# Optimization experiments

Measured on AMD Instinct MI355X. Metric: run time of the kernel, lower is better.

Reference implementation:

```python
import jax, jax.numpy as jnp
import numpy as np
from jax import lax

LEA, STE, GRA = 8, 8, 8
C_DIM = LEA + STE + GRA          # 24
AUX_DIM = 5
IN_DIM = C_DIM + AUX_DIM         # 29


def setup_inputs() -> dict:
    key = jax.random.key(0)
    ks = jax.random.split(key, 12)
    B, T = 1024, 366
    X = jax.random.uniform(ks[0], (B, T, 4), dtype=jnp.float32)
    ORY = jax.random.uniform(ks[1], (B, T, 7), dtype=jnp.float32)
    W_redis = jax.random.normal(ks[2], (C_DIM * C_DIM, IN_DIM), dtype=jnp.float32)
    b_redis = jax.random.normal(ks[3], (C_DIM * C_DIM,), dtype=jnp.float32)
    W_part = jax.random.normal(ks[4], (C_DIM, IN_DIM), dtype=jnp.float32)
    b_part = jax.random.normal(ks[5], (C_DIM,), dtype=jnp.float32)
    W_cons = jax.random.normal(ks[6], (C_DIM, IN_DIM), dtype=jnp.float32)
    b_cons = jax.random.normal(ks[7], (C_DIM,), dtype=jnp.float32)
    W_assim = jax.random.normal(ks[8], (1, IN_DIM), dtype=jnp.float32)
    b_assim = jax.random.normal(ks[9], (1,), dtype=jnp.float32)
    c2a_par = jnp.ones((C_DIM,), dtype=jnp.float32)
    g2y_par = jnp.ones((GRA,), dtype=jnp.float32)
    return dict(X=X, ORY=ORY, W_redis=W_redis, b_redis=b_redis,
                W_part=W_part, b_part=b_part, W_cons=W_cons, b_cons=b_cons,
                W_assim=W_assim, b_assim=b_assim, c2a_par=c2a_par, g2y_par=g2y_par)


def _redis_prior():
    # ones over C_cell part, zeros over aux except index -4 (rad) = 1
    p = jnp.concatenate([jnp.ones(C_DIM, jnp.float32), jnp.zeros(AUX_DIM, jnp.float32)])
    return p.at[IN_DIM - 4].set(1.0)


def _forward(X, ORY, W_redis, b_redis, W_part, b_part, W_cons, b_cons,
             W_assim, b_assim, c2a_par, g2y_par):
    B, T, _ = X.shape
    # ---- preprocessing ----
    N_cum = jnp.cumsum(X[:, :, 3], axis=-1)[..., None]          # [B,T,1]
    t_ave = jnp.mean(X[:, :, 1:3], axis=-1, keepdims=True)       # [B,T,1]
    dvs = ORY[:, :, :1]
    rad = X[:, :, 0:1]
    tmax = X[:, :, 1:2]
    tmin = X[:, :, 2:3]
    FRPAR = 0.5
    eff = 0.54 - (jnp.clip(t_ave * 50.0, 10.0, 40.0) - 10.0) / 30.0 * (0.54 - 0.36)
    R2C_par = (40000.0 / 20000.0) * FRPAR * eff / 3.6 * (12.0 / 44.0)
    C_potential = rad * R2C_par                                  # [B,T,1]
    AUX = jnp.concatenate([dvs, rad, tmax, tmin, N_cum], axis=-1)  # [B,T,5]

    redis_prior = _redis_prior()
    # all other input priors are ones, all output priors are zeros -> no-ops

    def redis_gate(x):
        z = (x * redis_prior) @ W_redis.T + b_redis
        return jax.nn.softmax(z.reshape(-1, C_DIM, C_DIM), axis=-1)

    def step(C_cell, ts):
        aux_t, cpot_t = ts                                       # [B,5], [B,1]
        x = jnp.concatenate([C_cell, aux_t], axis=1)             # [B,29]
        assim = jax.nn.sigmoid(x @ W_assim.T + b_assim)          # [B,1]
        part = jax.nn.softmax(x @ W_part.T + b_part, axis=-1)    # [B,24]
        cons = jax.nn.sigmoid(x @ W_cons.T + b_cons)             # [B,24]
        redis = redis_gate(x)                                    # [B,24,24]
        C_in = assim * cpot_t                                    # [B,1]
        C_cell = C_cell + C_in * part
        C_cell = C_cell * (1.0 - cons)
        C_cell = jnp.einsum('bi,bij->bj', C_cell, redis)
        x2 = jnp.concatenate([C_cell, aux_t], axis=1)
        redis2 = redis_gate(x2)
        C_conv = jnp.einsum('bi,bij->bj', C_cell, redis2)
        return C_cell, (C_cell, C_conv)

    aux_seq = jnp.transpose(AUX[:, :T - 1, :], (1, 0, 2))        # [T-1,B,5]
    cpot_seq = jnp.transpose(C_potential[:, :T - 1, :], (1, 0, 2))
    C0 = jnp.zeros((B, C_DIM), X.dtype)
    _, (C_all, C_conv_all) = lax.scan(step, C0, (aux_seq, cpot_seq))
    C_cell_all = jnp.transpose(C_all, (1, 0, 2))                 # [B,T-1,24]
    C_cell_convergence_all = jnp.transpose(C_conv_all, (1, 0, 2))

    pai = jnp.sum(jnp.abs(C_cell_all * c2a_par), axis=2, keepdims=True)
    lea = jnp.sum(C_cell_all[:, :, 0:LEA], axis=2, keepdims=True) / 0.419
    ste = jnp.sum(C_cell_all[:, :, LEA:LEA + STE], axis=2, keepdims=True) / 0.431
    gra = jnp.sum(C_cell_all[:, :, LEA + STE:C_DIM], axis=2, keepdims=True) / 0.487
    agb = lea + ste + gra
    yie = jnp.sum(jnp.abs(C_cell_all[:, :, LEA + STE:C_DIM] * g2y_par),
                  axis=2, keepdims=True) / 0.487
    all_day = jnp.concatenate([dvs[:, 1:], pai, lea, ste, gra, agb, yie], axis=2)
    all_day = jnp.concatenate([ORY[:, :1, :], all_day], axis=1)  # [B,T,7]
    return all_day, C_cell_all, C_cell_convergence_all


def reference(X, ORY, W_redis, b_redis, W_part, b_part, W_cons, b_cons,
              W_assim, b_assim, c2a_par, g2y_par):
    return _forward(X, ORY, W_redis, b_redis, W_part, b_part, W_cons, b_cons,
                    W_assim, b_assim, c2a_par, g2y_par)
```

## Files before the change

kernel.cpp:

```cpp
#include <hip/hip_runtime.h>

#define B_ 1024
#define T_ 366
#define NS_ 365
#define CD_ 24

__device__ __forceinline__ float sigm(float x) { return __fdividef(1.f, 1.f + __expf(-x)); }
__device__ __forceinline__ float rl(float v, int k) {
    return __int_as_float(__builtin_amdgcn_readlane(__float_as_int(v), k));
}

__global__ void mclstm_pack(const float* __restrict__ Wr, const float* __restrict__ br,
                            const float* __restrict__ Wp, const float* __restrict__ bp,
                            const float* __restrict__ Wc, const float* __restrict__ bc,
                            const float* __restrict__ Wa, const float* __restrict__ ba,
                            float* __restrict__ Wpk, float* __restrict__ Apk) {
    const int e = blockIdx.x * 64 + threadIdx.x;
    if (e < 576) {
#pragma unroll
        for (int k = 0; k < 24; ++k) Wpk[e * 32 + k] = Wr[e * 29 + k];
        Wpk[e * 32 + 24] = Wr[e * 29 + 25];
        Wpk[e * 32 + 25] = br[e];
#pragma unroll
        for (int k = 26; k < 32; ++k) Wpk[e * 32 + k] = 0.f;
    } else if (e < 625) {
        const int r = e - 576;
#pragma unroll
        for (int k = 0; k < 29; ++k)
            Apk[r * 32 + k] = (r < 24) ? Wp[r * 29 + k] : (r < 48) ? Wc[(r - 24) * 29 + k] : Wa[k];
        Apk[r * 32 + 29] = (r < 24) ? bp[r] : (r < 48) ? bc[r - 24] : ba[0];
        Apk[r * 32 + 30] = 0.f; Apk[r * 32 + 31] = 0.f;
    }
}

__global__ __attribute__((amdgpu_flat_work_group_size(128, 128), amdgpu_waves_per_eu(2, 2)))
void mclstm_main(const float* __restrict__ X, const float* __restrict__ ORY,
                 const float* __restrict__ Wpk, const float* __restrict__ Apk,
                 const float* __restrict__ c2a, const float* __restrict__ g2y,
                 float* __restrict__ allday, float* __restrict__ Ccell,
                 float* __restrict__ Cconv)
{
    __shared__ float zb1[600], zb2[600];
    __shared__ alignas(16) float pb1[672], pb2[672];
    __shared__ alignas(16) float cbuf[24];
    __shared__ float cmb[24];

    const int tid = threadIdx.x;
    const int l = tid & 63;
    const int wv = tid >> 6;
    const int b = blockIdx.x;

    float wrg[4][24], wrad[4], brg[4];
    int za[4];
#pragma unroll
    for (int j = 0; j < 4; ++j) {
        const int e = tid + 128 * j;
        const float4* wp = (const float4*)(Wpk + (size_t)e * 32);
#pragma unroll
        for (int q = 0; q < 6; ++q) {
            const float4 v = wp[q];
            wrg[j][4*q] = v.x; wrg[j][4*q+1] = v.y; wrg[j][4*q+2] = v.z; wrg[j][4*q+3] = v.w;
        }
        const float4 t = wp[6];
        wrad[j] = t.x; brg[j] = t.y;
        za[j] = (e / 24) * 25 + (e % 24);
    }
    float ext[32];
    {
        const float4* p = (const float4*)((wv == 0) ? (Wpk + (size_t)(512 + l) * 32)
                                                    : (Apk + (size_t)((l < 49) ? l : 48) * 32));
#pragma unroll
        for (int q = 0; q < 8; ++q) {
            const float4 v = p[q];
            ext[4*q] = v.x; ext[4*q+1] = v.y; ext[4*q+2] = v.z; ext[4*q+3] = v.w;
        }
    }
    const int za4 = ((512 + l) / 24) * 25 + ((512 + l) % 24);

    const bool even = ((l & 1) == 0) && (l < 48);
    const float c2 = even ? c2a[l >> 1] : 0.f;
    const float gy = (even && l >= 32) ? g2y[(l >> 1) - 16] : 0.f;

    const float* xrow = X + (size_t)b * T_ * 4;
    const float* orow = ORY + (size_t)b * T_ * 7;

    if (tid < 7) allday[(size_t)b * T_ * 7 + tid] = orow[tid];
    if (tid < 24) cbuf[tid] = 0.f;
    __syncthreads();

    float Ncum = 0.f, radp = 0.f;

    for (int u = 0; u <= NS_; ++u) {
        const bool do1 = (u < NS_), doCv = (u > 0);
        const int uu = do1 ? u : (NS_ - 1);
        const float rad = xrow[uu * 4 + 0];

        float Cs[24];
#pragma unroll
        for (int q = 0; q < 6; ++q) {
            const float4 v = ((const float4*)cbuf)[q];
            Cs[4*q] = v.x; Cs[4*q+1] = v.y; Cs[4*q+2] = v.z; Cs[4*q+3] = v.w;
        }

#pragma unroll
        for (int j = 0; j < 4; ++j) {
            float p0 = brg[j], p1 = 0.f, p2 = 0.f, p3 = 0.f;
#pragma unroll
            for (int k = 0; k < 24; k += 4) {
                p0 = fmaf(wrg[j][k],   Cs[k],   p0);
                p1 = fmaf(wrg[j][k+1], Cs[k+1], p1);
                p2 = fmaf(wrg[j][k+2], Cs[k+2], p2);
                p3 = fmaf(wrg[j][k+3], Cs[k+3], p3);
            }
            const float D = (p0 + p1) + (p2 + p3);
            if (do1)  zb1[za[j]] = fmaf(wrad[j], rad,  D);
            if (doCv) zb2[za[j]] = fmaf(wrad[j], radp, D);
        }

        if (wv == 0) {
            float p0 = ext[25], p1 = 0.f, p2 = 0.f, p3 = 0.f;
#pragma unroll
            for (int k = 0; k < 24; k += 4) {
                p0 = fmaf(ext[k],   Cs[k],   p0);
                p1 = fmaf(ext[k+1], Cs[k+1], p1);
                p2 = fmaf(ext[k+2], Cs[k+2], p2);
                p3 = fmaf(ext[k+3], Cs[k+3], p3);
            }
            const float D = (p0 + p1) + (p2 + p3);
            if (do1)  zb1[za4] = fmaf(ext[24], rad,  D);
            if (doCv) zb2[za4] = fmaf(ext[24], radp, D);
        } else if (do1) {
            const float tmx = xrow[uu * 4 + 1], tmn = xrow[uu * 4 + 2];
            Ncum += xrow[uu * 4 + 3];
            const float dvs = orow[uu * 7];
            const float tave = 0.5f * (tmx + tmn);
            const float clm = fminf(fmaxf(tave * 50.f, 10.f), 40.f);
            const float eff = 0.54f - (clm - 10.f) * (0.18f / 30.f);
            const float cpot = rad * (eff * (2.f * 0.5f / 3.6f * (12.f / 44.f)));

            float z = ext[29];
#pragma unroll
            for (int k = 0; k < 24; ++k) z = fmaf(ext[k], Cs[k], z);
            z = fmaf(ext[24], dvs, z);
            z = fmaf(ext[25], rad, z);
            z = fmaf(ext[26], tmx, z);
            z = fmaf(ext[27], tmn, z);
            z = fmaf(ext[28], Ncum, z);

            float pm = (l < 24) ? z : -1e30f;
#pragma unroll
            for (int o = 1; o < 32; o <<= 1) pm = fmaxf(pm, __shfl_xor(pm, o, 32));
            float pe = (l < 24) ? __expf(z - pm) : 0.f;
            float ps = pe;
#pragma unroll
            for (int o = 1; o < 32; o <<= 1) ps += __shfl_xor(ps, o, 32);
            const float conz = __shfl(z, 24 + (l & 31), 64);
            const float asmz = __shfl(z, 48, 64);
            if (l < 24) {
                const float part = __fdividef(pe, ps);
                const float cmv = cbuf[l];
                cmb[l] = (cmv + sigm(asmz) * cpot * part) * (1.f - sigm(conz));
            }
        }
        __syncthreads();

        {
            const bool act = (l < 48) && ((wv == 0) ? do1 : doCv);
            if (act) {
                const int r = l >> 1, h = l & 1;
                const float* zs = (wv == 0) ? zb1 : zb2;
                float* pd = (wv == 0) ? pb1 : pb2;
                float z[12];
#pragma unroll
                for (int i = 0; i < 12; ++i) z[i] = zs[r * 25 + h * 12 + i];
                float m = z[0];
#pragma unroll
                for (int i = 1; i < 12; ++i) m = fmaxf(m, z[i]);
                m = fmaxf(m, __shfl_xor(m, 1));
                float s = 0.f;
#pragma unroll
                for (int i = 0; i < 12; ++i) { z[i] = __expf(z[i] - m); s += z[i]; }
                s += __shfl_xor(s, 1);
                const float mlt = (wv == 0) ? cmb[r] : cbuf[r];
                const float f = __fdividef(mlt, s);
#pragma unroll
                for (int i = 0; i < 12; ++i) pd[(h * 12 + i) * 28 + r] = z[i] * f;
            }
        }
        __syncthreads();

        {
            const bool a0 = (wv == 0) && (l < 48) && do1;
            const bool a1 = (wv == 1) && (l < 48) && doCv;
            const int c = l >> 1, h = l & 1;
            float s = 0.f;
            if (a0 || a1) {
                const float* psrc = (wv == 0) ? pb1 : pb2;
                const float4* p4 = (const float4*)&psrc[c * 28 + h * 12];
#pragma unroll
                for (int i = 0; i < 3; ++i) {
                    const float4 v = p4[i];
                    s += (v.x + v.y) + (v.z + v.w);
                }
                s += __shfl_xor(s, 1);
            }
            if (a1 && h == 0) Cconv[((size_t)b * NS_ + (u - 1)) * CD_ + c] = s;
            if (a0 && h == 0) {
                cbuf[c] = s;
                Ccell[((size_t)b * NS_ + u) * CD_ + c] = s;
            }
            if (wv == 0 && do1) {
                const float cv = even ? s : 0.f;
                const float pv = fabsf(cv * c2);
                const float yv = fabsf(cv * gy);
                float a16 = cv, p16 = pv, y16 = yv;
#pragma unroll
                for (int o = 1; o < 16; o <<= 1) {
                    a16 += __shfl_xor(a16, o, 16);
                    p16 += __shfl_xor(p16, o, 16);
                    y16 += __shfl_xor(y16, o, 16);
                }
                const float pai = rl(p16, 0) + rl(p16, 16) + rl(p16, 32);
                const float lea = rl(a16, 0)  * (1.f / 0.419f);
                const float ste = rl(a16, 16) * (1.f / 0.431f);
                const float gra = rl(a16, 32) * (1.f / 0.487f);
                const float yie = rl(y16, 32) * (1.f / 0.487f);
                const float agb = lea + ste + gra;
                const float dvsn = orow[(u + 1) * 7];
                if (l < 7) {
                    float val = dvsn;
                    val = (l == 1) ? pai : val;
                    val = (l == 2) ? lea : val;
                    val = (l == 3) ? ste : val;
                    val = (l == 4) ? gra : val;
                    val = (l == 5) ? agb : val;
                    val = (l == 6) ? yie : val;
                    allday[((size_t)b * T_ + (u + 1)) * 7 + l] = val;
                }
            }
        }
        __syncthreads();
        radp = rad;
    }
}

extern "C" void kernel_launch(void* const* d_in, const int* in_sizes, int n_in,
                              void* d_out, int out_size, void* d_ws, size_t ws_size,
                              hipStream_t stream) {
    const float* X   = (const float*)d_in[0];
    const float* ORY = (const float*)d_in[1];
    const float* Wr  = (const float*)d_in[2];
    const float* br  = (const float*)d_in[3];
    const float* Wp  = (const float*)d_in[4];
    const float* bp  = (const float*)d_in[5];
    const float* Wc  = (const float*)d_in[6];
    const float* bc  = (const float*)d_in[7];
    const float* Wa  = (const float*)d_in[8];
    const float* ba  = (const float*)d_in[9];
    const float* c2a = (const float*)d_in[10];
    const float* g2y = (const float*)d_in[11];

    float* allday = (float*)d_out;
    float* Ccell  = allday + (size_t)B_ * T_ * 7;
    float* Cconv  = Ccell + (size_t)B_ * NS_ * CD_;

    float* Wpk = (float*)d_ws;
    float* Apk = Wpk + 576 * 32;

    hipLaunchKernelGGL(mclstm_pack, dim3(10), dim3(64), 0, stream,
                       Wr, br, Wp, bp, Wc, bc, Wa, ba, Wpk, Apk);
    hipLaunchKernelGGL(mclstm_main, dim3(B_), dim3(128), 0, stream,
                       X, ORY, Wpk, Apk, c2a, g2y, allday, Ccell, Cconv);
}
```

Measured before the change: 788.3 us.

## Process four batch rows per block with shared-memory weights and prefetched inputs

Each 512-thread block now handles four batch rows instead of one. The redistribution weights are staged once into swizzled LDS and reused across the four state vectors, so each weight read feeds four FMAs. Four waves compute the auxiliary softmax and gates per row, while the other four compute the 576-row matrix-vector products. X and ORY values for the next step are prefetched into registers, taking global loads off the serial step. The cost is fewer blocks (256), more LDS per block, heavier per-thread register use, and block-wide syncs across 8 waves on a latency-bound recurrence.

```diff
diff --git a/kernel.cpp b/kernel.cpp
--- a/kernel.cpp
+++ b/kernel.cpp
@@ -4,6 +4,7 @@
 #define T_ 366
 #define NS_ 365
 #define CD_ 24
+#define NCH 4
 
 __device__ __forceinline__ float sigm(float x) { return __fdividef(1.f, 1.f + __expf(-x)); }
 __device__ __forceinline__ float rl(float v, int k) {
@@ -33,184 +34,210 @@
     }
 }
 
-__global__ __attribute__((amdgpu_flat_work_group_size(128, 128), amdgpu_waves_per_eu(2, 2)))
-void mclstm_main(const float* __restrict__ X, const float* __restrict__ ORY,
-                 const float* __restrict__ Wpk, const float* __restrict__ Apk,
-                 const float* __restrict__ c2a, const float* __restrict__ g2y,
-                 float* __restrict__ allday, float* __restrict__ Ccell,
-                 float* __restrict__ Cconv)
+__global__ __launch_bounds__(512, 1) void mclstm_main(
+    const float* __restrict__ X, const float* __restrict__ ORY,
+    const float* __restrict__ Wpk, const float* __restrict__ Apk,
+    const float* __restrict__ c2a, const float* __restrict__ g2y,
+    float* __restrict__ allday, float* __restrict__ Ccell, float* __restrict__ Cconv)
 {
-    __shared__ float zb1[600], zb2[600];
-    __shared__ alignas(16) float pb1[672], pb2[672];
-    __shared__ alignas(16) float cbuf[24];
-    __shared__ float cmb[24];
+    __shared__ float4 Wl[576 * 8];
+    __shared__ float4 Al[49 * 8];
+    __shared__ float zb[NCH][2][600];
+    __shared__ __align__(16) float pb[NCH][2][672];
+    __shared__ __align__(16) float cbuf[NCH][24];
+    __shared__ float cmb[NCH][24];
+    __shared__ float rads[NCH];
+    __shared__ float dvsb[NCH];
 
     const int tid = threadIdx.x;
-    const int l = tid & 63;
-    const int wv = tid >> 6;
-    const int b = blockIdx.x;
-
-    float wrg[4][24], wrad[4], brg[4];
-    int za[4];
-#pragma unroll
-    for (int j = 0; j < 4; ++j) {
-        const int e = tid + 128 * j;
-        const float4* wp = (const float4*)(Wpk + (size_t)e * 32);
-#pragma unroll
-        for (int q = 0; q < 6; ++q) {
-            const float4 v = wp[q];
-            wrg[j][4*q] = v.x; wrg[j][4*q+1] = v.y; wrg[j][4*q+2] = v.z; wrg[j][4*q+3] = v.w;
-        }
-        const float4 t = wp[6];
-        wrad[j] = t.x; brg[j] = t.y;
-        za[j] = (e / 24) * 25 + (e % 24);
+    const int wv = tid >> 6, l = tid & 63;
+    const int b0 = blockIdx.x * NCH;
+
+    for (int g = tid; g < 576 * 8; g += 512) {
+        const int e = g >> 3, q = g & 7;
+        Wl[e * 8 + (q ^ (e & 7))] = ((const float4*)Wpk)[g];
     }
-    float ext[32];
-    {
-        const float4* p = (const float4*)((wv == 0) ? (Wpk + (size_t)(512 + l) * 32)
-                                                    : (Apk + (size_t)((l < 49) ? l : 48) * 32));
-#pragma unroll
-        for (int q = 0; q < 8; ++q) {
-            const float4 v = p[q];
-            ext[4*q] = v.x; ext[4*q+1] = v.y; ext[4*q+2] = v.z; ext[4*q+3] = v.w;
-        }
+    for (int g = tid; g < 49 * 8; g += 512) {
+        const int e = g >> 3, q = g & 7;
+        Al[e * 8 + (q ^ (e & 7))] = ((const float4*)Apk)[g];
     }
-    const int za4 = ((512 + l) / 24) * 25 + ((512 + l) % 24);
-
-    const bool even = ((l & 1) == 0) && (l < 48);
-    const float c2 = even ? c2a[l >> 1] : 0.f;
-    const float gy = (even && l >= 32) ? g2y[(l >> 1) - 16] : 0.f;
-
-    const float* xrow = X + (size_t)b * T_ * 4;
-    const float* orow = ORY + (size_t)b * T_ * 7;
-
-    if (tid < 7) allday[(size_t)b * T_ * 7 + tid] = orow[tid];
-    if (tid < 24) cbuf[tid] = 0.f;
+    if (tid < NCH * 24) ((float*)cbuf)[tid] = 0.f;
+    if (tid < NCH) rads[tid] = X[(size_t)(b0 + tid) * T_ * 4];
+    if (wv < NCH && l < 7)
+        allday[(size_t)(b0 + wv) * T_ * 7 + l] = ORY[(size_t)(b0 + wv) * T_ * 7 + l];
+
+    const bool isAux = (wv < 4);
+    const int j = wv & 3;
+    const float* xj = X + (size_t)(b0 + j) * T_ * 4;
+    const float* oj = ORY + (size_t)(b0 + j) * T_ * 7;
+
+    const int jBC = wv >> 1, kBC = wv & 1;
+    const int rc = l >> 1, hh = l & 1;
+
+    const bool evn = ((l & 1) == 0) && (l < 48);
+    const float c2 = (kBC == 0 && evn) ? c2a[l >> 1] : 0.f;
+    const float gy = (kBC == 0 && evn && l >= 32) ? g2y[(l >> 1) - 16] : 0.f;
+
+    const int s = tid - 256;
+    const int e1 = s, e2 = s + 256;
+    const bool has3 = (!isAux) && ((l & 3) == 0);
+    const int e3 = 512 + ((wv - 4) << 4) + (l >> 2);
+    const int za1 = (e1 / 24) * 25 + e1 % 24;
+    const int za2 = (e2 / 24) * 25 + e2 % 24;
+    const int za3 = (e3 / 24) * 25 + e3 % 24;
+
+    float4 cur = make_float4(0.f, 0.f, 0.f, 0.f);
+    float dcur = 0.f;
+    if (isAux) { cur = *(const float4*)xj; dcur = oj[0]; }
+
     __syncthreads();
 
-    float Ncum = 0.f, radp = 0.f;
+    float Ncum = 0.f;
+    float rp0 = 0.f, rp1 = 0.f, rp2 = 0.f, rp3 = 0.f;
 
     for (int u = 0; u <= NS_; ++u) {
         const bool do1 = (u < NS_), doCv = (u > 0);
-        const int uu = do1 ? u : (NS_ - 1);
-        const float rad = xrow[uu * 4 + 0];
-
-        float Cs[24];
-#pragma unroll
-        for (int q = 0; q < 6; ++q) {
-            const float4 v = ((const float4*)cbuf)[q];
-            Cs[4*q] = v.x; Cs[4*q+1] = v.y; Cs[4*q+2] = v.z; Cs[4*q+3] = v.w;
-        }
-
-#pragma unroll
-        for (int j = 0; j < 4; ++j) {
-            float p0 = brg[j], p1 = 0.f, p2 = 0.f, p3 = 0.f;
-#pragma unroll
-            for (int k = 0; k < 24; k += 4) {
-                p0 = fmaf(wrg[j][k],   Cs[k],   p0);
-                p1 = fmaf(wrg[j][k+1], Cs[k+1], p1);
-                p2 = fmaf(wrg[j][k+2], Cs[k+2], p2);
-                p3 = fmaf(wrg[j][k+3], Cs[k+3], p3);
-            }
-            const float D = (p0 + p1) + (p2 + p3);
-            if (do1)  zb1[za[j]] = fmaf(wrad[j], rad,  D);
-            if (doCv) zb2[za[j]] = fmaf(wrad[j], radp, D);
-        }
-
-        if (wv == 0) {
-            float p0 = ext[25], p1 = 0.f, p2 = 0.f, p3 = 0.f;
-#pragma unroll
-            for (int k = 0; k < 24; k += 4) {
-                p0 = fmaf(ext[k],   Cs[k],   p0);
-                p1 = fmaf(ext[k+1], Cs[k+1], p1);
-                p2 = fmaf(ext[k+2], Cs[k+2], p2);
-                p3 = fmaf(ext[k+3], Cs[k+3], p3);
-            }
-            const float D = (p0 + p1) + (p2 + p3);
-            if (do1)  zb1[za4] = fmaf(ext[24], rad,  D);
-            if (doCv) zb2[za4] = fmaf(ext[24], radp, D);
-        } else if (do1) {
-            const float tmx = xrow[uu * 4 + 1], tmn = xrow[uu * 4 + 2];
-            Ncum += xrow[uu * 4 + 3];
-            const float dvs = orow[uu * 7];
-            const float tave = 0.5f * (tmx + tmn);
-            const float clm = fminf(fmaxf(tave * 50.f, 10.f), 40.f);
-            const float eff = 0.54f - (clm - 10.f) * (0.18f / 30.f);
-            const float cpot = rad * (eff * (2.f * 0.5f / 3.6f * (12.f / 44.f)));
-
-            float z = ext[29];
-#pragma unroll
-            for (int k = 0; k < 24; ++k) z = fmaf(ext[k], Cs[k], z);
-            z = fmaf(ext[24], dvs, z);
-            z = fmaf(ext[25], rad, z);
-            z = fmaf(ext[26], tmx, z);
-            z = fmaf(ext[27], tmn, z);
-            z = fmaf(ext[28], Ncum, z);
-
-            float pm = (l < 24) ? z : -1e30f;
-#pragma unroll
-            for (int o = 1; o < 32; o <<= 1) pm = fmaxf(pm, __shfl_xor(pm, o, 32));
-            float pe = (l < 24) ? __expf(z - pm) : 0.f;
-            float ps = pe;
-#pragma unroll
-            for (int o = 1; o < 32; o <<= 1) ps += __shfl_xor(ps, o, 32);
-            const float conz = __shfl(z, 24 + (l & 31), 64);
-            const float asmz = __shfl(z, 48, 64);
-            if (l < 24) {
-                const float part = __fdividef(pe, ps);
-                const float cmv = cbuf[l];
-                cmb[l] = (cmv + sigm(asmz) * cpot * part) * (1.f - sigm(conz));
-            }
+        const float ra0 = rads[0], ra1 = rads[1], ra2 = rads[2], ra3 = rads[3];
+
+        float4 nxt = cur; float dn = dcur;
+
+        if (isAux) {
+            const int un = (u + 1 <= NS_) ? (u + 1) : NS_;
+            nxt = *(const float4*)(xj + un * 4);
+            dn = oj[un * 7];
+            if (do1) {
+                float Csa[24];
+#pragma unroll
+                for (int q = 0; q < 6; ++q) {
+                    const float4 v = ((const float4*)cbuf[j])[q];
+                    Csa[4*q] = v.x; Csa[4*q+1] = v.y; Csa[4*q+2] = v.z; Csa[4*q+3] = v.w;
+                }
+                Ncum += cur.w;
+                const float tave = 0.5f * (cur.y + cur.z);
+                const float clm = fminf(fmaxf(tave * 50.f, 10.f), 40.f);
+                const float eff = 0.54f - (clm - 10.f) * (0.18f / 30.f);
+                const float cpot = cur.x * (eff * (2.f * 0.5f / 3.6f * (12.f / 44.f)));
+
+                const int ar = (l < 49) ? l : 48;
+                float au[32];
+#pragma unroll
+                for (int q = 0; q < 8; ++q) {
+                    const float4 v = Al[ar * 8 + (q ^ (ar & 7))];
+                    au[4*q] = v.x; au[4*q+1] = v.y; au[4*q+2] = v.z; au[4*q+3] = v.w;
+                }
+                float z = au[29];
+#pragma unroll
+                for (int k = 0; k < 24; ++k) z = fmaf(au[k], Csa[k], z);
+                z = fmaf(au[24], dcur, z);
+                z = fmaf(au[25], cur.x, z);
+                z = fmaf(au[26], cur.y, z);
+                z = fmaf(au[27], cur.z, z);
+                z = fmaf(au[28], Ncum, z);
+
+                float pm = (l < 24) ? z : -1e30f;
+#pragma unroll
+                for (int o = 1; o < 32; o <<= 1) pm = fmaxf(pm, __shfl_xor(pm, o, 32));
+                float pe = (l < 24) ? __expf(z - pm) : 0.f;
+                float ps = pe;
+#pragma unroll
+                for (int o = 1; o < 32; o <<= 1) ps += __shfl_xor(ps, o, 32);
+                const float conz = __shfl(z, 24 + (l & 31), 64);
+                const float asmz = __shfl(z, 48, 64);
+                if (l < 24) {
+                    const float part = __fdividef(pe, ps);
+                    cmb[j][l] = (Csa[l] + sigm(asmz) * cpot * part) * (1.f - sigm(conz));
+                }
+            }
+        } else {
+            float Cs0[24], Cs1[24], Cs2[24], Cs3[24];
+#pragma unroll
+            for (int q = 0; q < 6; ++q) {
+                const float4 v0 = ((const float4*)cbuf[0])[q];
+                const float4 v1 = ((const float4*)cbuf[1])[q];
+                const float4 v2 = ((const float4*)cbuf[2])[q];
+                const float4 v3 = ((const float4*)cbuf[3])[q];
+                Cs0[4*q]=v0.x; Cs0[4*q+1]=v0.y; Cs0[4*q+2]=v0.z; Cs0[4*q+3]=v0.w;
+                Cs1[4*q]=v1.x; Cs1[4*q+1]=v1.y; Cs1[4*q+2]=v1.z; Cs1[4*q+3]=v1.w;
+                Cs2[4*q]=v2.x; Cs2[4*q+1]=v2.y; Cs2[4*q+2]=v2.z; Cs2[4*q+3]=v2.w;
+                Cs3[4*q]=v3.x; Cs3[4*q+1]=v3.y; Cs3[4*q+2]=v3.z; Cs3[4*q+3]=v3.w;
+            }
+#define ROW(E, ZA)                                                             \
+            {                                                                  \
+                float w[28];                                                   \
+                _Pragma("unroll") for (int q = 0; q < 7; ++q) {                \
+                    const float4 v = Wl[(E) * 8 + (q ^ ((E) & 7))];            \
+                    w[4*q]=v.x; w[4*q+1]=v.y; w[4*q+2]=v.z; w[4*q+3]=v.w;      \
+                }                                                              \
+                float D0 = w[25], D1 = w[25], D2 = w[25], D3 = w[25];          \
+                _Pragma("unroll") for (int k = 0; k < 24; ++k) {               \
+                    D0 = fmaf(w[k], Cs0[k], D0); D1 = fmaf(w[k], Cs1[k], D1);  \
+                    D2 = fmaf(w[k], Cs2[k], D2); D3 = fmaf(w[k], Cs3[k], D3);  \
+                }                                                              \
+                if (do1) {                                                     \
+                    zb[0][0][ZA] = fmaf(w[24], ra0, D0);                       \
+                    zb[1][0][ZA] = fmaf(w[24], ra1, D1);                       \
+                    zb[2][0][ZA] = fmaf(w[24], ra2, D2);                       \
+                    zb[3][0][ZA] = fmaf(w[24], ra3, D3);                       \
+                }                                                              \
+                if (doCv) {                                                    \
+                    zb[0][1][ZA] = fmaf(w[24], rp0, D0);                       \
+                    zb[1][1][ZA] = fmaf(w[24], rp1, D1);                       \
+                    zb[2][1][ZA] = fmaf(w[24], rp2, D2);                       \
+                    zb[3][1][ZA] = fmaf(w[24], rp3, D3);                       \
+                }                                                              \
+            }
+            ROW(e1, za1)
+            ROW(e2, za2)
+            if (has3) ROW(e3, za3)
+#undef ROW
         }
         __syncthreads();
 
         {
-            const bool act = (l < 48) && ((wv == 0) ? do1 : doCv);
+            const bool act = (l < 48) && (kBC ? doCv : do1);
             if (act) {
-                const int r = l >> 1, h = l & 1;
-                const float* zs = (wv == 0) ? zb1 : zb2;
-                float* pd = (wv == 0) ? pb1 : pb2;
                 float z[12];
 #pragma unroll
-                for (int i = 0; i < 12; ++i) z[i] = zs[r * 25 + h * 12 + i];
+                for (int i = 0; i < 12; ++i) z[i] = zb[jBC][kBC][rc * 25 + hh * 12 + i];
                 float m = z[0];
 #pragma unroll
                 for (int i = 1; i < 12; ++i) m = fmaxf(m, z[i]);
                 m = fmaxf(m, __shfl_xor(m, 1));
-                float s = 0.f;
-#pragma unroll
-                for (int i = 0; i < 12; ++i) { z[i] = __expf(z[i] - m); s += z[i]; }
-                s += __shfl_xor(s, 1);
-                const float mlt = (wv == 0) ? cmb[r] : cbuf[r];
-                const float f = __fdividef(mlt, s);
-#pragma unroll
-                for (int i = 0; i < 12; ++i) pd[(h * 12 + i) * 28 + r] = z[i] * f;
-            }
+                float ss = 0.f;
+#pragma unroll
+                for (int i = 0; i < 12; ++i) { z[i] = __expf(z[i] - m); ss += z[i]; }
+                ss += __shfl_xor(ss, 1);
+                const float mlt = kBC ? cbuf[jBC][rc] : cmb[jBC][rc];
+                const float f = __fdividef(mlt, ss);
+#pragma unroll
+                for (int i = 0; i < 12; ++i) pb[jBC][kBC][(hh * 12 + i) * 28 + rc] = z[i] * f;
+            }
+            if (isAux && l == 0) { rads[j] = nxt.x; dvsb[j] = dn; }
         }
         __syncthreads();
 
         {
-            const bool a0 = (wv == 0) && (l < 48) && do1;
-            const bool a1 = (wv == 1) && (l < 48) && doCv;
-            const int c = l >> 1, h = l & 1;
-            float s = 0.f;
-            if (a0 || a1) {
-                const float* psrc = (wv == 0) ? pb1 : pb2;
-                const float4* p4 = (const float4*)&psrc[c * 28 + h * 12];
+            const bool act = (l < 48) && (kBC ? doCv : do1);
+            float ssum = 0.f;
+            if (act) {
+                const float4* p4 = (const float4*)&pb[jBC][kBC][rc * 28 + hh * 12];
 #pragma unroll
                 for (int i = 0; i < 3; ++i) {
                     const float4 v = p4[i];
-                    s += (v.x + v.y) + (v.z + v.w);
-                }
-                s += __shfl_xor(s, 1);
-            }
-            if (a1 && h == 0) Cconv[((size_t)b * NS_ + (u - 1)) * CD_ + c] = s;
-            if (a0 && h == 0) {
-                cbuf[c] = s;
-                Ccell[((size_t)b * NS_ + u) * CD_ + c] = s;
-            }
-            if (wv == 0 && do1) {
-                const float cv = even ? s : 0.f;
+                    ssum += (v.x + v.y) + (v.z + v.w);
+                }
+                ssum += __shfl_xor(ssum, 1);
+                if (hh == 0) {
+                    if (kBC) {
+                        Cconv[((size_t)(b0 + jBC) * NS_ + (u - 1)) * CD_ + rc] = ssum;
+                    } else {
+                        cbuf[jBC][rc] = ssum;
+                        Ccell[((size_t)(b0 + jBC) * NS_ + u) * CD_ + rc] = ssum;
+                    }
+                }
+            }
+            if (kBC == 0 && do1) {
+                const float cv = evn ? ssum : 0.f;
                 const float pv = fabsf(cv * c2);
                 const float yv = fabsf(cv * gy);
                 float a16 = cv, p16 = pv, y16 = yv;
@@ -226,7 +253,7 @@
                 const float gra = rl(a16, 32) * (1.f / 0.487f);
                 const float yie = rl(y16, 32) * (1.f / 0.487f);
                 const float agb = lea + ste + gra;
-                const float dvsn = orow[(u + 1) * 7];
+                const float dvsn = dvsb[jBC];
                 if (l < 7) {
                     float val = dvsn;
                     val = (l == 1) ? pai : val;
@@ -235,12 +262,13 @@
                     val = (l == 4) ? gra : val;
                     val = (l == 5) ? agb : val;
                     val = (l == 6) ? yie : val;
-                    allday[((size_t)b * T_ + (u + 1)) * 7 + l] = val;
+                    allday[((size_t)(b0 + jBC) * T_ + (u + 1)) * 7 + l] = val;
                 }
             }
         }
         __syncthreads();
-        radp = rad;
+        if (isAux) { cur = nxt; dcur = dn; }
+        rp0 = ra0; rp1 = ra1; rp2 = ra2; rp3 = ra3;
     }
 }
 
@@ -269,6 +297,6 @@
 
     hipLaunchKernelGGL(mclstm_pack, dim3(10), dim3(64), 0, stream,
                        Wr, br, Wp, bp, Wc, bc, Wa, ba, Wpk, Apk);
-    hipLaunchKernelGGL(mclstm_main, dim3(B_), dim3(128), 0, stream,
+    hipLaunchKernelGGL(mclstm_main, dim3(B_ / NCH), dim3(512), 0, stream,
                        X, ORY, Wpk, Apk, c2a, g2y, allday, Ccell, Cconv);
 }
```

Measured after the change: 983.9 us. 24.8% more time.

## Merge softmax and reduction phases per wave, prefetch next-step inputs, pad z buffer

Applied to the files above, without the earlier changes.

Folds the softmax-redistribution phase and the column-sum phase into one block, so each wave writes and reads back only its own pb buffer. This removes one __syncthreads per time step from the serial recurrence. The next step's X row and dvs are now loaded one iteration ahead to hide global-load latency. The z buffers are padded to a row stride of 28 so each lane can read its 12 values as float4. The merged phase relies on LDS ordering within a single wave, since no barrier now separates the transposed write from the read-back.

```diff
diff --git a/kernel.cpp b/kernel.cpp
--- a/kernel.cpp
+++ b/kernel.cpp
@@ -40,14 +40,13 @@
                  float* __restrict__ allday, float* __restrict__ Ccell,
                  float* __restrict__ Cconv)
 {
-    __shared__ float zb1[600], zb2[600];
-    __shared__ alignas(16) float pb1[672], pb2[672];
-    __shared__ alignas(16) float cbuf[24];
+    __shared__ __align__(16) float zb1[672], zb2[672];
+    __shared__ __align__(16) float pb1[672], pb2[672];
+    __shared__ __align__(16) float cbuf[24];
     __shared__ float cmb[24];
 
     const int tid = threadIdx.x;
-    const int l = tid & 63;
-    const int wv = tid >> 6;
+    const int l = tid & 63, wv = tid >> 6;
     const int b = blockIdx.x;
 
     float wrg[4][24], wrad[4], brg[4];
@@ -63,7 +62,7 @@
         }
         const float4 t = wp[6];
         wrad[j] = t.x; brg[j] = t.y;
-        za[j] = (e / 24) * 25 + (e % 24);
+        za[j] = (e / 24) * 28 + (e % 24);
     }
     float ext[32];
     {
@@ -75,11 +74,12 @@
             ext[4*q] = v.x; ext[4*q+1] = v.y; ext[4*q+2] = v.z; ext[4*q+3] = v.w;
         }
     }
-    const int za4 = ((512 + l) / 24) * 25 + ((512 + l) % 24);
-
-    const bool even = ((l & 1) == 0) && (l < 48);
-    const float c2 = even ? c2a[l >> 1] : 0.f;
-    const float gy = (even && l >= 32) ? g2y[(l >> 1) - 16] : 0.f;
+    const int za4 = ((512 + l) / 24) * 28 + (512 + l) % 24;
+
+    const int rc = l >> 1, hh = l & 1;
+    const bool evn = ((l & 1) == 0) && (l < 48);
+    const float c2 = evn ? c2a[l >> 1] : 0.f;
+    const float gy = (evn && l >= 32) ? g2y[(l >> 1) - 16] : 0.f;
 
     const float* xrow = X + (size_t)b * T_ * 4;
     const float* orow = ORY + (size_t)b * T_ * 7;
@@ -88,12 +88,18 @@
     if (tid < 24) cbuf[tid] = 0.f;
     __syncthreads();
 
-    float Ncum = 0.f, radp = 0.f;
+    float Ncum = 0.f, rp = 0.f;
+    float4 xc = *(const float4*)xrow;
+    float dvsc = orow[0];
 
     for (int u = 0; u <= NS_; ++u) {
         const bool do1 = (u < NS_), doCv = (u > 0);
-        const int uu = do1 ? u : (NS_ - 1);
-        const float rad = xrow[uu * 4 + 0];
+
+        const int un = (u + 1 <= NS_) ? (u + 1) : NS_;
+        const float4 xn = *(const float4*)(xrow + un * 4);
+        const float dn = orow[un * 7];
+
+        const float ra = xc.x;
 
         float Cs[24];
 #pragma unroll
@@ -101,6 +107,7 @@
             const float4 v = ((const float4*)cbuf)[q];
             Cs[4*q] = v.x; Cs[4*q+1] = v.y; Cs[4*q+2] = v.z; Cs[4*q+3] = v.w;
         }
+        const float mlt1 = cbuf[rc];
 
 #pragma unroll
         for (int j = 0; j < 4; ++j) {
@@ -113,8 +120,8 @@
                 p3 = fmaf(wrg[j][k+3], Cs[k+3], p3);
             }
             const float D = (p0 + p1) + (p2 + p3);
-            if (do1)  zb1[za[j]] = fmaf(wrad[j], rad,  D);
-            if (doCv) zb2[za[j]] = fmaf(wrad[j], radp, D);
+            if (do1)  zb1[za[j]] = fmaf(wrad[j], ra, D);
+            if (doCv) zb2[za[j]] = fmaf(wrad[j], rp, D);
         }
 
         if (wv == 0) {
@@ -127,24 +134,22 @@
                 p3 = fmaf(ext[k+3], Cs[k+3], p3);
             }
             const float D = (p0 + p1) + (p2 + p3);
-            if (do1)  zb1[za4] = fmaf(ext[24], rad,  D);
-            if (doCv) zb2[za4] = fmaf(ext[24], radp, D);
+            if (do1)  zb1[za4] = fmaf(ext[24], ra, D);
+            if (doCv) zb2[za4] = fmaf(ext[24], rp, D);
         } else if (do1) {
-            const float tmx = xrow[uu * 4 + 1], tmn = xrow[uu * 4 + 2];
-            Ncum += xrow[uu * 4 + 3];
-            const float dvs = orow[uu * 7];
-            const float tave = 0.5f * (tmx + tmn);
+            Ncum += xc.w;
+            const float tave = 0.5f * (xc.y + xc.z);
             const float clm = fminf(fmaxf(tave * 50.f, 10.f), 40.f);
             const float eff = 0.54f - (clm - 10.f) * (0.18f / 30.f);
-            const float cpot = rad * (eff * (2.f * 0.5f / 3.6f * (12.f / 44.f)));
+            const float cpot = ra * (eff * (2.f * 0.5f / 3.6f * (12.f / 44.f)));
 
             float z = ext[29];
 #pragma unroll
             for (int k = 0; k < 24; ++k) z = fmaf(ext[k], Cs[k], z);
-            z = fmaf(ext[24], dvs, z);
-            z = fmaf(ext[25], rad, z);
-            z = fmaf(ext[26], tmx, z);
-            z = fmaf(ext[27], tmn, z);
+            z = fmaf(ext[24], dvsc, z);
+            z = fmaf(ext[25], ra, z);
+            z = fmaf(ext[26], xc.y, z);
+            z = fmaf(ext[27], xc.z, z);
             z = fmaf(ext[28], Ncum, z);
 
             float pm = (l < 24) ? z : -1e30f;
@@ -158,89 +163,84 @@
             const float asmz = __shfl(z, 48, 64);
             if (l < 24) {
                 const float part = __fdividef(pe, ps);
-                const float cmv = cbuf[l];
-                cmb[l] = (cmv + sigm(asmz) * cpot * part) * (1.f - sigm(conz));
+                cmb[l] = (cbuf[l] + sigm(asmz) * cpot * part) * (1.f - sigm(conz));
             }
         }
         __syncthreads();
 
+        float ssum = 0.f;
         {
-            const bool act = (l < 48) && ((wv == 0) ? do1 : doCv);
+            const bool act = (l < 48) && (wv ? doCv : do1);
             if (act) {
-                const int r = l >> 1, h = l & 1;
-                const float* zs = (wv == 0) ? zb1 : zb2;
-                float* pd = (wv == 0) ? pb1 : pb2;
+                const float* zs = wv ? zb2 : zb1;
+                float* pbk = wv ? pb2 : pb1;
+                const float4* z4 = (const float4*)(zs + rc * 28 + hh * 12);
                 float z[12];
 #pragma unroll
-                for (int i = 0; i < 12; ++i) z[i] = zs[r * 25 + h * 12 + i];
+                for (int q = 0; q < 3; ++q) {
+                    const float4 v = z4[q];
+                    z[4*q] = v.x; z[4*q+1] = v.y; z[4*q+2] = v.z; z[4*q+3] = v.w;
+                }
                 float m = z[0];
 #pragma unroll
                 for (int i = 1; i < 12; ++i) m = fmaxf(m, z[i]);
                 m = fmaxf(m, __shfl_xor(m, 1));
-                float s = 0.f;
-#pragma unroll
-                for (int i = 0; i < 12; ++i) { z[i] = __expf(z[i] - m); s += z[i]; }
-                s += __shfl_xor(s, 1);
-                const float mlt = (wv == 0) ? cmb[r] : cbuf[r];
-                const float f = __fdividef(mlt, s);
-#pragma unroll
-                for (int i = 0; i < 12; ++i) pd[(h * 12 + i) * 28 + r] = z[i] * f;
-            }
-        }
-        __syncthreads();
-
-        {
-            const bool a0 = (wv == 0) && (l < 48) && do1;
-            const bool a1 = (wv == 1) && (l < 48) && doCv;
-            const int c = l >> 1, h = l & 1;
-            float s = 0.f;
-            if (a0 || a1) {
-                const float* psrc = (wv == 0) ? pb1 : pb2;
-                const float4* p4 = (const float4*)&psrc[c * 28 + h * 12];
+                float ss = 0.f;
+#pragma unroll
+                for (int i = 0; i < 12; ++i) { z[i] = __expf(z[i] - m); ss += z[i]; }
+                ss += __shfl_xor(ss, 1);
+                const float mult = wv ? mlt1 : cmb[rc];
+                const float f = __fdividef(mult, ss);
+#pragma unroll
+                for (int i = 0; i < 12; ++i) pbk[(hh * 12 + i) * 28 + rc] = z[i] * f;
+
+                const float4* p4 = (const float4*)(pbk + rc * 28 + hh * 12);
 #pragma unroll
                 for (int i = 0; i < 3; ++i) {
                     const float4 v = p4[i];
-                    s += (v.x + v.y) + (v.z + v.w);
+                    ssum += (v.x + v.y) + (v.z + v.w);
                 }
-                s += __shfl_xor(s, 1);
-            }
-            if (a1 && h == 0) Cconv[((size_t)b * NS_ + (u - 1)) * CD_ + c] = s;
-            if (a0 && h == 0) {
-                cbuf[c] = s;
-                Ccell[((size_t)b * NS_ + u) * CD_ + c] = s;
-            }
-            if (wv == 0 && do1) {
-                const float cv = even ? s : 0.f;
-                const float pv = fabsf(cv * c2);
-                const float yv = fabsf(cv * gy);
-                float a16 = cv, p16 = pv, y16 = yv;
-#pragma unroll
-                for (int o = 1; o < 16; o <<= 1) {
-                    a16 += __shfl_xor(a16, o, 16);
-                    p16 += __shfl_xor(p16, o, 16);
-                    y16 += __shfl_xor(y16, o, 16);
+                ssum += __shfl_xor(ssum, 1);
+                if (hh == 0) {
+                    if (wv) {
+                        Cconv[((size_t)b * NS_ + (u - 1)) * CD_ + rc] = ssum;
+                    } else {
+                        cbuf[rc] = ssum;
+                        Ccell[((size_t)b * NS_ + u) * CD_ + rc] = ssum;
+                    }
                 }
-                const float pai = rl(p16, 0) + rl(p16, 16) + rl(p16, 32);
-                const float lea = rl(a16, 0)  * (1.f / 0.419f);
-                const float ste = rl(a16, 16) * (1.f / 0.431f);
-                const float gra = rl(a16, 32) * (1.f / 0.487f);
-                const float yie = rl(y16, 32) * (1.f / 0.487f);
-                const float agb = lea + ste + gra;
-                const float dvsn = orow[(u + 1) * 7];
-                if (l < 7) {
-                    float val = dvsn;
-                    val = (l == 1) ? pai : val;
-                    val = (l == 2) ? lea : val;
-                    val = (l == 3) ? ste : val;
-                    val = (l == 4) ? gra : val;
-                    val = (l == 5) ? agb : val;
-                    val = (l == 6) ? yie : val;
-                    allday[((size_t)b * T_ + (u + 1)) * 7 + l] = val;
-                }
+            }
+        }
+        if (wv == 0 && do1) {
+            const float cv = evn ? ssum : 0.f;
+            const float pv = fabsf(cv * c2);
+            const float yv = fabsf(cv * gy);
+            float a16 = cv, p16 = pv, y16 = yv;
+#pragma unroll
+            for (int o = 1; o < 16; o <<= 1) {
+                a16 += __shfl_xor(a16, o, 16);
+                p16 += __shfl_xor(p16, o, 16);
+                y16 += __shfl_xor(y16, o, 16);
+            }
+            const float pai = rl(p16, 0) + rl(p16, 16) + rl(p16, 32);
+            const float lea = rl(a16, 0)  * (1.f / 0.419f);
+            const float ste = rl(a16, 16) * (1.f / 0.431f);
+            const float gra = rl(a16, 32) * (1.f / 0.487f);
+            const float yie = rl(y16, 32) * (1.f / 0.487f);
+            const float agb = lea + ste + gra;
+            if (l < 7) {
+                float val = dn;
+                val = (l == 1) ? pai : val;
+                val = (l == 2) ? lea : val;
+                val = (l == 3) ? ste : val;
+                val = (l == 4) ? gra : val;
+                val = (l == 5) ? agb : val;
+                val = (l == 6) ? yie : val;
+                allday[((size_t)b * T_ + (u + 1)) * 7 + l] = val;
             }
         }
         __syncthreads();
-        radp = rad;
+        rp = ra; xc = xn; dvsc = dn;
     }
 }
 
```

New measurement: 731.3 us. 1.08x faster.
